# Optimization experiments

Hardware: AMD Instinct MI355X
Metric: run time of the kernel (lower is better)

Reference implementation:

```python
import jax, jax.numpy as jnp
import numpy as np
from jax.scipy.special import ndtri

NUM_BITS = 4
BLOCK_SIZE = 64
OUT_F, IN_F = 4096, 4096


def _nf_table(num_bits=NUM_BITS):
    # Faithful to NFQuantizer.create_normal_map (asymmetric branch)
    offset = 0.9677083
    variations = 2 ** num_bits
    v1 = ndtri(jnp.linspace(offset, 0.5, variations // 2 + 1, dtype=jnp.float32)[:-1])
    v3 = -ndtri(jnp.linspace(offset, 0.5, variations // 2, dtype=jnp.float32)[:-1])
    v = jnp.concatenate([v1, jnp.zeros((1,), jnp.float32), v3])
    v = jnp.sort(v)
    return v / v.max()


def setup_inputs() -> dict:
    key = jax.random.key(0)
    k1, k2, k3, k4, k5 = jax.random.split(key, 5)
    x = jax.random.normal(k1, (8192, IN_F), dtype=jnp.float32)
    qweight = jax.random.randint(k2, (IN_F * OUT_F // 2, 1), 0, 256, dtype=jnp.int32)
    absmax = jax.random.uniform(k3, (IN_F * OUT_F // BLOCK_SIZE, 1), dtype=jnp.float32) * 0.1 + 1e-3
    lora_A = jax.random.normal(k4, (64, IN_F), dtype=jnp.float32) * 0.02
    lora_B = jax.random.normal(k5, (OUT_F, 64), dtype=jnp.float32) * 0.02
    return {"x": x, "qweight": qweight, "absmax": absmax, "lora_A": lora_A, "lora_B": lora_B}


def reference(x, qweight, absmax, lora_A, lora_B):
    table = _nf_table()
    q = qweight[:, 0]
    # dequantize_block: low nibble first (i=0), then high nibble (i=1)
    idx = jnp.stack([q & 0xF, (q >> NUM_BITS) & 0xF], axis=-1)  # [Q, 2]
    w = table[idx].reshape(-1, BLOCK_SIZE) * absmax             # [n_blocks, block_size]
    w = w.reshape(OUT_F, IN_F)
    dense = x @ w.T
    lora = (x @ lora_A.T) @ lora_B.T
    return dense + lora
```

## Files before the change

### kernel.cpp

```cpp
#include <hip/hip_runtime.h>

#define IN_F 4096
#define OUT_F 4096
#define M_ROWS 8192
#define GK 4096

typedef float  floatx4 __attribute__((ext_vector_type(4)));
typedef short  shortx8 __attribute__((ext_vector_type(8)));

__device__ __forceinline__ unsigned short f2bf(float f) {
    unsigned int u = __float_as_uint(f);
    u = (u + 0x7FFFu + ((u >> 16) & 1u)) >> 16;
    return (unsigned short)u;
}

__device__ __forceinline__ float bf2f(unsigned short u) {
    return __uint_as_float((unsigned)u << 16);
}

__constant__ float NF4_TAB[16] = {
    -1.0f, -0.6961928009986877f, -0.5250730514526367f, -0.39491748809814453f,
    -0.28444138169288635f, -0.18477343022823334f, -0.09105003625154495f, 0.0f,
    0.07958029955625534f, 0.16093020141124725f, 0.2461123913526535f, 0.33791524171829224f,
    0.44070982933044434f, 0.5626170039176941f, 0.7229568362236023f, 1.0f
};

__device__ __forceinline__ void gll16(const void* g, void* l) {
    __builtin_amdgcn_global_load_lds(
        (const __attribute__((address_space(1))) void*)g,
        (__attribute__((address_space(3))) void*)l, 16, 0, 0);
}

__global__ __launch_bounds__(256) void prep(
    const float* __restrict__ A, const float* __restrict__ Bm,
    const float* __restrict__ x,
    short* __restrict__ At, short* __restrict__ Bb, short* __restrict__ Xb)
{
    __shared__ float tile[64][65];
    const int b = blockIdx.x;
    const int t = threadIdx.x;

    if (b < 64) {
        const int ib = b * 64;
        const int r = t >> 2, c0 = (t & 3) * 16;
        #pragma unroll
        for (int k = 0; k < 4; ++k) {
            float4 v = *(const float4*)(A + (size_t)r * IN_F + ib + c0 + k * 4);
            tile[r][c0 + k * 4 + 0] = v.x;
            tile[r][c0 + k * 4 + 1] = v.y;
            tile[r][c0 + k * 4 + 2] = v.z;
            tile[r][c0 + k * 4 + 3] = v.w;
        }
        __syncthreads();
        const int i = t >> 2, r0 = (t & 3) * 16;
        union { unsigned short u[8]; int4 v; } p0, p1;
        #pragma unroll
        for (int k = 0; k < 8; ++k) p0.u[k] = f2bf(tile[r0 + k][i]);
        #pragma unroll
        for (int k = 0; k < 8; ++k) p1.u[k] = f2bf(tile[r0 + 8 + k][i]);
        *(int4*)(At + (size_t)(ib + i) * 64 + r0)     = p0.v;
        *(int4*)(At + (size_t)(ib + i) * 64 + r0 + 8) = p1.v;
    } else if (b < 192) {
        const size_t i = ((size_t)(b - 64) * 256 + t) * 8;
        float4 a = *(const float4*)(Bm + i);
        float4 c = *(const float4*)(Bm + i + 4);
        union { unsigned short u[8]; int4 v; } p;
        p.u[0] = f2bf(a.x); p.u[1] = f2bf(a.y); p.u[2] = f2bf(a.z); p.u[3] = f2bf(a.w);
        p.u[4] = f2bf(c.x); p.u[5] = f2bf(c.y); p.u[6] = f2bf(c.z); p.u[7] = f2bf(c.w);
        *(int4*)(Bb + i) = p.v;
    } else {
        const size_t i = ((size_t)(b - 192) * 256 + t) * 8;
        float4 a = *(const float4*)(x + i);
        float4 c = *(const float4*)(x + i + 4);
        union { unsigned short u[8]; int4 v; } p;
        p.u[0] = f2bf(a.x); p.u[1] = f2bf(a.y); p.u[2] = f2bf(a.z); p.u[3] = f2bf(a.w);
        p.u[4] = f2bf(c.x); p.u[5] = f2bf(c.y); p.u[6] = f2bf(c.z); p.u[7] = f2bf(c.w);
        *(int4*)(Xb + i) = p.v;
    }
}

#define BM 128
#define BN 128

__global__ __launch_bounds__(256) void lora_weff(
    const short* __restrict__ Bb,
    const short* __restrict__ At,
    const int*   __restrict__ qw,
    const float* __restrict__ absmax,
    short*       __restrict__ W)
{
    __shared__ union SMem {
        struct { short As[BM * 32]; short Bs[BN * 32]; } mm;
        short Wt[128 * 136];
    } sm;
    __shared__ float nf4s[16];

    const int tid  = threadIdx.x;
    const int lane = tid & 63;
    const int wave = tid >> 6;
    const int bn = blockIdx.x * BN;
    const int bm = blockIdx.y * BM;

    if (tid < 16) nf4s[tid] = NF4_TAB[tid];

    const int r_o = tid >> 1;
    const int h   = tid & 1;
    const int go  = bm + r_o;
    const int* qbase = qw + (size_t)go * 2048 + (bn >> 1) + h * 32;
    int4 q4[8];
    #pragma unroll
    for (int k = 0; k < 8; ++k) q4[k] = *(const int4*)(qbase + 4 * k);
    const float am = absmax[(size_t)go * 64 + (bn >> 6) + h];

    const int ar = tid >> 2;
    const int ac = ((tid & 3) ^ ((ar >> 1) & 3)) * 8;
    const short* gA0 = Bb + (size_t)(bm + ar) * 64 + ac;
    const short* gA1 = gA0 + (size_t)64 * 64;
    const short* gB0 = At + (size_t)(bn + ar) * 64 + ac;
    const short* gB1 = gB0 + (size_t)64 * 64;
    short* lA0 = sm.mm.As + tid * 8;
    short* lA1 = sm.mm.As + 2048 + tid * 8;
    short* lB0 = sm.mm.Bs + tid * 8;
    short* lB1 = sm.mm.Bs + 2048 + tid * 8;

    const int wm = (wave >> 1) * 64;
    const int wn = (wave & 1) * 64;
    const int fr = lane & 15;
    const int qd = lane >> 4;
    const int fk_sw = (((lane >> 4) ^ ((fr >> 1) & 3))) * 8;

    floatx4 zero = {0.f, 0.f, 0.f, 0.f};
    floatx4 acc[4][4];
    #pragma unroll
    for (int i = 0; i < 4; ++i)
        #pragma unroll
        for (int j = 0; j < 4; ++j) acc[i][j] = zero;

    #pragma unroll
    for (int kt = 0; kt < 2; ++kt) {
        gll16(gA0, lA0);
        gll16(gA1, lA1);
        gll16(gB0, lB0);
        gll16(gB1, lB1);
        gA0 += 32; gA1 += 32; gB0 += 32; gB1 += 32;
        __syncthreads();

        shortx8 af[4], bfr[4];
        #pragma unroll
        for (int i = 0; i < 4; ++i) {
            af[i]  = *(const shortx8*)&sm.mm.As[(wm + i * 16 + fr) * 32 + fk_sw];
            bfr[i] = *(const shortx8*)&sm.mm.Bs[(wn + i * 16 + fr) * 32 + fk_sw];
        }
        #pragma unroll
        for (int i = 0; i < 4; ++i)
            #pragma unroll
            for (int j = 0; j < 4; ++j)
                acc[i][j] = __builtin_amdgcn_mfma_f32_16x16x32_bf16(
                    af[i], bfr[j], acc[i][j], 0, 0, 0);
        __syncthreads();
    }

    #pragma unroll
    for (int i = 0; i < 4; ++i) {
        const int r0 = wm + i * 16 + qd * 4;
        #pragma unroll
        for (int j = 0; j < 4; ++j) {
            const int c = wn + j * 16 + fr;
            union { unsigned short u[4]; uint2 v; } p;
            p.u[0] = f2bf(acc[i][j][0]);
            p.u[1] = f2bf(acc[i][j][1]);
            p.u[2] = f2bf(acc[i][j][2]);
            p.u[3] = f2bf(acc[i][j][3]);
            *(uint2*)&sm.Wt[c * 136 + r0] = p.v;
        }
    }
    __syncthreads();

    short* out = W + (size_t)go * IN_F + bn + h * 64;
    #pragma unroll
    for (int k = 0; k < 8; ++k) {
        const int qs[4] = { q4[k].x, q4[k].y, q4[k].z, q4[k].w };
        union { unsigned short u[8]; int4 v; } p;
        #pragma unroll
        for (int d = 0; d < 4; ++d) {
            const int q = qs[d];
            const int c = h * 64 + k * 8 + d * 2;
            const float l0 = bf2f((unsigned short)sm.Wt[c * 136 + r_o]);
            const float l1 = bf2f((unsigned short)sm.Wt[(c + 1) * 136 + r_o]);
            p.u[2 * d]     = f2bf(fmaf(nf4s[q & 15],        am, l0));
            p.u[2 * d + 1] = f2bf(fmaf(nf4s[(q >> 4) & 15], am, l1));
        }
        *(int4*)(out + k * 8) = p.v;
    }
}

#define BM2 256
#define BN2 256
#define BK2 64
#define NT2 (GK / BK2)

#define MFMA16(a, b, c) __builtin_amdgcn_mfma_f32_16x16x32_bf16((a), (b), (c), 0, 0, 0)
#define SBAR()  __builtin_amdgcn_s_barrier()
#define SFEN()  __builtin_amdgcn_sched_barrier(0)

__global__ __launch_bounds__(512, 2) void gemm_bt2(
    const short* __restrict__ Xb,
    const short* __restrict__ Wb,
    float*       __restrict__ C)
{
    __shared__ short lds[2 * 32768];

    const int tid  = threadIdx.x;
    const int lane = tid & 63;
    const int wave = tid >> 6;
    const int bn = blockIdx.x * BN2;
    const int bm = blockIdx.y * BM2;

    const int wm = (wave >> 2) * 128;
    const int wn = (wave & 3) * 64;
    const int fr = lane & 15;
    const int qd = lane >> 4;
    const int rsw = fr & 7;
    const int kof[2] = { ((0 * 4 + qd) ^ rsw) << 3, ((1 * 4 + qd) ^ rsw) << 3 };

    const int srow = tid >> 3;
    const int gch  = (tid & 7) ^ (srow & 7);
    const short* pA = Xb + (size_t)(bm + srow) * GK + gch * 8;
    const short* pB = Wb + (size_t)(bn + srow) * GK + gch * 8;

    auto STAGE = [&](const short* P, int matOff, int h, int t, int buf) {
        short* d = lds + buf * 32768 + matOff + h * 8192 + tid * 8;
        const short* s = P + (size_t)(h * 128) * GK + (size_t)t * BK2;
        gll16(s, d);
        gll16(s + (size_t)64 * GK, d + 4096);
    };

    floatx4 zero = {0.f, 0.f, 0.f, 0.f};
    floatx4 acc[8][4];
    #pragma unroll
    for (int i = 0; i < 8; ++i)
        #pragma unroll
        for (int j = 0; j < 4; ++j) acc[i][j] = zero;

    STAGE(pA, 0,     0, 0, 0);
    STAGE(pA, 0,     1, 0, 0);
    STAGE(pB, 16384, 0, 0, 0);
    STAGE(pB, 16384, 1, 0, 0);
    STAGE(pA, 0,     0, 1, 1);
    STAGE(pB, 16384, 0, 1, 1);
    STAGE(pB, 16384, 1, 1, 1);
    asm volatile("s_waitcnt vmcnt(6)" ::: "memory");
    SBAR();
    SFEN();

    for (int t = 0; t < NT2; ++t) {
        const int cur = t & 1;
        const short* Ah = lds + cur * 32768 + (wm >> 7) * 8192;
        const short* Bh = lds + cur * 32768 + 16384 + (wn >> 7) * 8192;
        const int bs = wn & 64;

        shortx8 af[4][2], bf[4][2];

        #pragma unroll
        for (int i = 0; i < 4; ++i) {
            af[i][0] = *(const shortx8*)(Ah + (i * 16 + fr) * 64 + kof[0]);
            af[i][1] = *(const shortx8*)(Ah + (i * 16 + fr) * 64 + kof[1]);
        }
        #pragma unroll
        for (int j = 0; j < 2; ++j) {
            bf[j][0] = *(const shortx8*)(Bh + (bs + j * 16 + fr) * 64 + kof[0]);
            bf[j][1] = *(const shortx8*)(Bh + (bs + j * 16 + fr) * 64 + kof[1]);
        }
        if (t + 1 < NT2) STAGE(pA, 0, 1, t + 1, cur ^ 1);
        SFEN();
        asm volatile("s_waitcnt lgkmcnt(0)" ::: "memory");
        SFEN();
        __builtin_amdgcn_s_setprio(1);
        #pragma unroll
        for (int i = 0; i < 4; ++i)
            #pragma unroll
            for (int j = 0; j < 2; ++j) {
                acc[i][j] = MFMA16(af[i][0], bf[j][0], acc[i][j]);
                acc[i][j] = MFMA16(af[i][1], bf[j][1], acc[i][j]);
            }
        __builtin_amdgcn_s_setprio(0);
        SFEN();
        SBAR();
        SFEN();

        #pragma unroll
        for (int j = 0; j < 2; ++j) {
            bf[2 + j][0] = *(const shortx8*)(Bh + (bs + (2 + j) * 16 + fr) * 64 + kof[0]);
            bf[2 + j][1] = *(const shortx8*)(Bh + (bs + (2 + j) * 16 + fr) * 64 + kof[1]);
        }
        SFEN();
        asm volatile("s_waitcnt lgkmcnt(0)" ::: "memory");
        SFEN();
        __builtin_amdgcn_s_setprio(1);
        #pragma unroll
        for (int i = 0; i < 4; ++i)
            #pragma unroll
            for (int j = 2; j < 4; ++j) {
                acc[i][j] = MFMA16(af[i][0], bf[j][0], acc[i][j]);
                acc[i][j] = MFMA16(af[i][1], bf[j][1], acc[i][j]);
            }
        __builtin_amdgcn_s_setprio(0);
        SFEN();
        SBAR();
        SFEN();

        #pragma unroll
        for (int i = 0; i < 4; ++i) {
            af[i][0] = *(const shortx8*)(Ah + (64 + i * 16 + fr) * 64 + kof[0]);
            af[i][1] = *(const shortx8*)(Ah + (64 + i * 16 + fr) * 64 + kof[1]);
        }
        if (t + 2 < NT2) {
            STAGE(pB, 16384, 0, t + 2, cur);
            STAGE(pB, 16384, 1, t + 2, cur);
        }
        SFEN();
        asm volatile("s_waitcnt lgkmcnt(0)" ::: "memory");
        SFEN();
        __builtin_amdgcn_s_setprio(1);
        #pragma unroll
        for (int i = 0; i < 4; ++i)
            #pragma unroll
            for (int j = 2; j < 4; ++j) {
                acc[4 + i][j] = MFMA16(af[i][0], bf[j][0], acc[4 + i][j]);
                acc[4 + i][j] = MFMA16(af[i][1], bf[j][1], acc[4 + i][j]);
            }
        __builtin_amdgcn_s_setprio(0);
        SFEN();
        SBAR();
        SFEN();

        if (t + 2 < NT2) STAGE(pA, 0, 0, t + 2, cur);
        SFEN();
        __builtin_amdgcn_s_setprio(1);
        #pragma unroll
        for (int i = 0; i < 4; ++i)
            #pragma unroll
            for (int j = 0; j < 2; ++j) {
                acc[4 + i][j] = MFMA16(af[i][0], bf[j][0], acc[4 + i][j]);
                acc[4 + i][j] = MFMA16(af[i][1], bf[j][1], acc[4 + i][j]);
            }
        __builtin_amdgcn_s_setprio(0);
        SFEN();
        if (t < NT2 - 2) {
            asm volatile("s_waitcnt vmcnt(6)" ::: "memory");
        } else if (t == NT2 - 2) {
            asm volatile("s_waitcnt vmcnt(0)" ::: "memory");
        }
        SBAR();
        SFEN();
    }

    const int row0 = bm + wm + qd * 4;
    const int col0 = bn + wn + fr;
    #pragma unroll
    for (int i = 0; i < 8; ++i)
        #pragma unroll
        for (int j = 0; j < 4; ++j) {
            float* cp = C + (size_t)(row0 + i * 16) * OUT_F + col0 + j * 16;
            #pragma unroll
            for (int rr = 0; rr < 4; ++rr)
                cp[(size_t)rr * OUT_F] = acc[i][j][rr];
        }
}

extern "C" void kernel_launch(void* const* d_in, const int* in_sizes, int n_in,
                              void* d_out, int out_size, void* d_ws, size_t ws_size,
                              hipStream_t stream) {
    const float* x  = (const float*)d_in[0];
    const int*   qw = (const int*)d_in[1];
    const float* am = (const float*)d_in[2];
    const float* lA = (const float*)d_in[3];
    const float* lB = (const float*)d_in[4];
    float* out = (float*)d_out;

    short* Weff = (short*)d_ws;
    short* Xb   = (short*)((char*)d_ws + (size_t)OUT_F * IN_F * 2);
    short* At   = (short*)((char*)d_ws + (size_t)(OUT_F * IN_F + M_ROWS * IN_F) * 2);
    short* Bb   = At + (size_t)IN_F * 64;

    prep<<<192 + (M_ROWS * IN_F) / 2048, 256, 0, stream>>>(lA, lB, x, At, Bb, Xb);
    lora_weff<<<dim3(IN_F / 128, OUT_F / 128), 256, 0, stream>>>(Bb, At, qw, am, Weff);
    gemm_bt2<<<dim3(OUT_F / BN2, M_ROWS / BM2), 512, 0, stream>>>(Xb, Weff, out);
}
```

Measured before the change: 478.3 us.

## Move x bf16 conversion into lora_weff launch and merge GEMM phases

The fp32-to-bf16 conversion of x moves out of the prep kernel and into extra blocks of the lora_weff launch, using a 1D grid. The intent is to overlap that bandwidth-bound conversion with the weight dequant/LoRA work and shorten the prep launch. Separately, the main GEMM loop goes from four MFMA phases per k-tile to two, loading all four B fragments at once and issuing the A staging alongside the B staging. This cuts barriers and waitcnts per tile but raises register pressure and reduces how finely loads are interleaved with math.

After: 466.4 us. 1.03x faster.

```diff
diff --git a/kernel.cpp b/kernel.cpp
--- a/kernel.cpp
+++ b/kernel.cpp
@@ -33,8 +33,7 @@
 
 __global__ __launch_bounds__(256) void prep(
     const float* __restrict__ A, const float* __restrict__ Bm,
-    const float* __restrict__ x,
-    short* __restrict__ At, short* __restrict__ Bb, short* __restrict__ Xb)
+    short* __restrict__ At, short* __restrict__ Bb)
 {
     __shared__ float tile[64][65];
     const int b = blockIdx.x;
@@ -60,7 +59,7 @@
         for (int k = 0; k < 8; ++k) p1.u[k] = f2bf(tile[r0 + 8 + k][i]);
         *(int4*)(At + (size_t)(ib + i) * 64 + r0)     = p0.v;
         *(int4*)(At + (size_t)(ib + i) * 64 + r0 + 8) = p1.v;
-    } else if (b < 192) {
+    } else {
         const size_t i = ((size_t)(b - 64) * 256 + t) * 8;
         float4 a = *(const float4*)(Bm + i);
         float4 c = *(const float4*)(Bm + i + 4);
@@ -68,14 +67,6 @@
         p.u[0] = f2bf(a.x); p.u[1] = f2bf(a.y); p.u[2] = f2bf(a.z); p.u[3] = f2bf(a.w);
         p.u[4] = f2bf(c.x); p.u[5] = f2bf(c.y); p.u[6] = f2bf(c.z); p.u[7] = f2bf(c.w);
         *(int4*)(Bb + i) = p.v;
-    } else {
-        const size_t i = ((size_t)(b - 192) * 256 + t) * 8;
-        float4 a = *(const float4*)(x + i);
-        float4 c = *(const float4*)(x + i + 4);
-        union { unsigned short u[8]; int4 v; } p;
-        p.u[0] = f2bf(a.x); p.u[1] = f2bf(a.y); p.u[2] = f2bf(a.z); p.u[3] = f2bf(a.w);
-        p.u[4] = f2bf(c.x); p.u[5] = f2bf(c.y); p.u[6] = f2bf(c.z); p.u[7] = f2bf(c.w);
-        *(int4*)(Xb + i) = p.v;
     }
 }
 
@@ -87,8 +78,22 @@
     const short* __restrict__ At,
     const int*   __restrict__ qw,
     const float* __restrict__ absmax,
-    short*       __restrict__ W)
+    short*       __restrict__ W,
+    const float* __restrict__ xin,
+    short*       __restrict__ Xb)
 {
+    const int b = blockIdx.x;
+    if (b >= 1024) {
+        const size_t i = ((size_t)(b - 1024) * 256 + threadIdx.x) * 8;
+        float4 a = *(const float4*)(xin + i);
+        float4 c = *(const float4*)(xin + i + 4);
+        union { unsigned short u[8]; int4 v; } p;
+        p.u[0] = f2bf(a.x); p.u[1] = f2bf(a.y); p.u[2] = f2bf(a.z); p.u[3] = f2bf(a.w);
+        p.u[4] = f2bf(c.x); p.u[5] = f2bf(c.y); p.u[6] = f2bf(c.z); p.u[7] = f2bf(c.w);
+        *(int4*)(Xb + i) = p.v;
+        return;
+    }
+
     __shared__ union SMem {
         struct { short As[BM * 32]; short Bs[BN * 32]; } mm;
         short Wt[128 * 136];
@@ -98,8 +103,8 @@
     const int tid  = threadIdx.x;
     const int lane = tid & 63;
     const int wave = tid >> 6;
-    const int bn = blockIdx.x * BN;
-    const int bm = blockIdx.y * BM;
+    const int bn = (b & 31) * BN;
+    const int bm = (b >> 5) * BM;
 
     if (tid < 16) nf4s[tid] = NF4_TAB[tid];
 
@@ -267,7 +272,7 @@
             af[i][1] = *(const shortx8*)(Ah + (i * 16 + fr) * 64 + kof[1]);
         }
         #pragma unroll
-        for (int j = 0; j < 2; ++j) {
+        for (int j = 0; j < 4; ++j) {
             bf[j][0] = *(const shortx8*)(Bh + (bs + j * 16 + fr) * 64 + kof[0]);
             bf[j][1] = *(const shortx8*)(Bh + (bs + j * 16 + fr) * 64 + kof[1]);
         }
@@ -279,7 +284,7 @@
         #pragma unroll
         for (int i = 0; i < 4; ++i)
             #pragma unroll
-            for (int j = 0; j < 2; ++j) {
+            for (int j = 0; j < 4; ++j) {
                 acc[i][j] = MFMA16(af[i][0], bf[j][0], acc[i][j]);
                 acc[i][j] = MFMA16(af[i][1], bf[j][1], acc[i][j]);
             }
@@ -289,27 +294,6 @@
         SFEN();
 
         #pragma unroll
-        for (int j = 0; j < 2; ++j) {
-            bf[2 + j][0] = *(const shortx8*)(Bh + (bs + (2 + j) * 16 + fr) * 64 + kof[0]);
-            bf[2 + j][1] = *(const shortx8*)(Bh + (bs + (2 + j) * 16 + fr) * 64 + kof[1]);
-        }
-        SFEN();
-        asm volatile("s_waitcnt lgkmcnt(0)" ::: "memory");
-        SFEN();
-        __builtin_amdgcn_s_setprio(1);
-        #pragma unroll
-        for (int i = 0; i < 4; ++i)
-            #pragma unroll
-            for (int j = 2; j < 4; ++j) {
-                acc[i][j] = MFMA16(af[i][0], bf[j][0], acc[i][j]);
-                acc[i][j] = MFMA16(af[i][1], bf[j][1], acc[i][j]);
-            }
-        __builtin_amdgcn_s_setprio(0);
-        SFEN();
-        SBAR();
-        SFEN();
-
-        #pragma unroll
         for (int i = 0; i < 4; ++i) {
             af[i][0] = *(const shortx8*)(Ah + (64 + i * 16 + fr) * 64 + kof[0]);
             af[i][1] = *(const shortx8*)(Ah + (64 + i * 16 + fr) * 64 + kof[1]);
@@ -317,6 +301,7 @@
         if (t + 2 < NT2) {
             STAGE(pB, 16384, 0, t + 2, cur);
             STAGE(pB, 16384, 1, t + 2, cur);
+            STAGE(pA, 0,     0, t + 2, cur);
         }
         SFEN();
         asm volatile("s_waitcnt lgkmcnt(0)" ::: "memory");
@@ -325,22 +310,7 @@
         #pragma unroll
         for (int i = 0; i < 4; ++i)
             #pragma unroll
-            for (int j = 2; j < 4; ++j) {
-                acc[4 + i][j] = MFMA16(af[i][0], bf[j][0], acc[4 + i][j]);
-                acc[4 + i][j] = MFMA16(af[i][1], bf[j][1], acc[4 + i][j]);
-            }
-        __builtin_amdgcn_s_setprio(0);
-        SFEN();
-        SBAR();
-        SFEN();
-
-        if (t + 2 < NT2) STAGE(pA, 0, 0, t + 2, cur);
-        SFEN();
-        __builtin_amdgcn_s_setprio(1);
-        #pragma unroll
-        for (int i = 0; i < 4; ++i)
-            #pragma unroll
-            for (int j = 0; j < 2; ++j) {
+            for (int j = 0; j < 4; ++j) {
                 acc[4 + i][j] = MFMA16(af[i][0], bf[j][0], acc[4 + i][j]);
                 acc[4 + i][j] = MFMA16(af[i][1], bf[j][1], acc[4 + i][j]);
             }
@@ -383,7 +353,8 @@
     short* At   = (short*)((char*)d_ws + (size_t)(OUT_F * IN_F + M_ROWS * IN_F) * 2);
     short* Bb   = At + (size_t)IN_F * 64;
 
-    prep<<<192 + (M_ROWS * IN_F) / 2048, 256, 0, stream>>>(lA, lB, x, At, Bb, Xb);
-    lora_weff<<<dim3(IN_F / 128, OUT_F / 128), 256, 0, stream>>>(Bb, At, qw, am, Weff);
+    prep<<<192, 256, 0, stream>>>(lA, lB, At, Bb);
+    lora_weff<<<1024 + (M_ROWS * IN_F) / 2048, 256, 0, stream>>>(
+        Bb, At, qw, am, Weff, x, Xb);
     gemm_bt2<<<dim3(OUT_F / BN2, M_ROWS / BM2), 512, 0, stream>>>(Xb, Weff, out);
 }
```
